# Kernel optimization log

Hardware: AMD Instinct MI355X
Metric: run time of the kernel (lower is better)

The kernel has to match this reference:

```python
import jax, jax.numpy as jnp
import numpy as np


def hard_sigmoid(x):
    # Theano/Keras hard_sigmoid: clip(0.2*x + 0.5, 0, 1)
    return jnp.clip(0.2 * x + 0.5, 0.0, 1.0)


def setup_inputs() -> dict:
    key = jax.random.key(0)
    ks = jax.random.split(key, 5)
    B, T, D, H = 64, 2048, 256, 128
    X = jax.random.normal(ks[0], (B, T, D), dtype=jnp.float32)
    W = jax.random.normal(ks[1], (D, H), dtype=jnp.float32) * 0.05
    U = jax.random.normal(ks[2], (H, H), dtype=jnp.float32) * (1.0 / np.sqrt(H))
    b = jnp.zeros((H,), dtype=jnp.float32)
    W_gate = jax.random.normal(ks[3], (D, H), dtype=jnp.float32) * 0.05
    b_gate = jnp.zeros((H,), dtype=jnp.float32)
    U_gate = jax.random.normal(ks[4], (H, H), dtype=jnp.float32) * (1.0 / np.sqrt(H))
    return {"X": X, "W": W, "U": U, "b": b,
            "W_gate": W_gate, "b_gate": b_gate, "U_gate": U_gate}


def reference(X, W, U, b, W_gate, b_gate, U_gate):
    # Precompute input projections for all timesteps (as the Theano code does)
    xx = jnp.einsum('btd,dh->bth', X, W) + b          # [B,T,H]
    xg = jnp.einsum('btd,dh->bth', X, W_gate) + b_gate  # [B,T,H]
    B, T, H = xx.shape

    def step(h, inp):
        xx_t, xg_t = inp                      # [B,H] each
        z = hard_sigmoid(xx_t + h @ U)        # update gate
        z_gate = jnp.tanh((xg_t * h) @ U_gate)
        z_out = jax.nn.softplus(h * z_gate)
        h_t = z * z_out + (1.0 - z) * h
        return h_t, None

    h0 = jnp.zeros((B, H), dtype=X.dtype)
    # scan over time: [T,B,H]
    h_final, _ = jax.lax.scan(step, h0, (jnp.swapaxes(xx, 0, 1), jnp.swapaxes(xg, 0, 1)))
    return h_final  # [B,H] (return_sequences=False -> last hidden state)
```

## Files before the change

### kernel.cpp

```cpp
#include <hip/hip_runtime.h>
#include <math.h>

#define B_ 64
#define T_ 2048
#define D_ 256
#define H_ 128

__device__ __forceinline__ float rlane(float v, int l) {
    return __int_as_float(__builtin_amdgcn_readlane(__float_as_int(v), l));
}
__device__ __forceinline__ float hard_sig(float x) {
    return fminf(fmaxf(fmaf(x, 0.2f, 0.5f), 0.0f), 1.0f);
}
__device__ __forceinline__ float fast_tanh(float x) {
    float ax = fabsf(x);
    float e  = __expf(-2.0f * ax);
    float r  = (1.0f - e) / (1.0f + e);
    return copysignf(r, x);
}
__device__ __forceinline__ float softplus_f(float x) {
    float ax = fabsf(x);
    return fmaxf(x, 0.0f) + __logf(1.0f + __expf(-ax));
}

__global__ __launch_bounds__(256) void proj_kernel(
    const float* __restrict__ X, const float* __restrict__ W,
    const float* __restrict__ Wg, const float* __restrict__ bias,
    const float* __restrict__ biasg, float* __restrict__ xxw,
    float* __restrict__ xgw, int t0, int Tc)
{
    const int tid = threadIdx.x;
    const int tx  = tid & 31;
    const int ty  = tid >> 5;
    const long rowbase = (long)blockIdx.x * 64;
    const int  b      = (int)(rowbase / Tc);
    const int  ttbase = (int)(rowbase % Tc);
    const float* xbase = X + ((long)b * T_ + t0 + ttbase) * D_;

    float accx[8][4];
    float accg[8][4];
#pragma unroll
    for (int r = 0; r < 8; ++r)
#pragma unroll
        for (int c = 0; c < 4; ++c) { accx[r][c] = 0.f; accg[r][c] = 0.f; }

    for (int k = 0; k < D_; k += 4) {
        float wA[4][4], wG[4][4];
#pragma unroll
        for (int kk = 0; kk < 4; ++kk) {
            float4 tw = *(const float4*)&W [(long)(k + kk) * H_ + tx * 4];
            float4 tg = *(const float4*)&Wg[(long)(k + kk) * H_ + tx * 4];
            wA[kk][0] = tw.x; wA[kk][1] = tw.y; wA[kk][2] = tw.z; wA[kk][3] = tw.w;
            wG[kk][0] = tg.x; wG[kk][1] = tg.y; wG[kk][2] = tg.z; wG[kk][3] = tg.w;
        }
#pragma unroll
        for (int r = 0; r < 8; ++r) {
            float4 xv = *(const float4*)&xbase[(long)(ty * 8 + r) * D_ + k];
            float xr[4] = {xv.x, xv.y, xv.z, xv.w};
#pragma unroll
            for (int c = 0; c < 4; ++c)
#pragma unroll
                for (int kk = 0; kk < 4; ++kk) {
                    accx[r][c] = fmaf(xr[kk], wA[kk][c], accx[r][c]);
                    accg[r][c] = fmaf(xr[kk], wG[kk][c], accg[r][c]);
                }
        }
    }

    float4 bj  = *(const float4*)&bias [tx * 4];
    float4 bgj = *(const float4*)&biasg[tx * 4];
#pragma unroll
    for (int r = 0; r < 8; ++r) {
        long row = rowbase + ty * 8 + r;
        float4 ox, og;
        ox.x = accx[r][0] + bj.x;  ox.y = accx[r][1] + bj.y;
        ox.z = accx[r][2] + bj.z;  ox.w = accx[r][3] + bj.w;
        og.x = accg[r][0] + bgj.x; og.y = accg[r][1] + bgj.y;
        og.z = accg[r][2] + bgj.z; og.w = accg[r][3] + bgj.w;
        *(float4*)&xxw[row * H_ + tx * 4] = ox;
        *(float4*)&xgw[row * H_ + tx * 4] = og;
    }
}

__global__ __launch_bounds__(512) void scan_kernel(
    const float* __restrict__ xxw, const float* __restrict__ xgw,
    const float* __restrict__ U, const float* __restrict__ Ug,
    float* __restrict__ hstate, float* __restrict__ hout,
    int t0, int Tc)
{
    const int tid    = threadIdx.x;
    const int j      = tid & 127;
    const int q      = tid >> 7;
    const int lane31 = tid & 31;
    const int i0     = q * 32;
    const int b      = blockIdx.x;

    __shared__ float hl[128];
    __shared__ float zp_l[4][128];
    __shared__ float gp_l[4][128];

    float Ureg[32], Ugreg[32];
#pragma unroll
    for (int i = 0; i < 32; ++i) {
        Ureg[i]  = U [(long)(i0 + i) * H_ + j];
        Ugreg[i] = Ug[(long)(i0 + i) * H_ + j];
    }

    const float* xxb = xxw + (long)b * Tc * H_;
    const float* xgb = xgw + (long)b * Tc * H_;

    float h0 = (t0 == 0) ? 0.0f : hstate[b * H_ + j];
    float hcur = h0;
    if (q == 0) hl[j] = h0;
    __syncthreads();

    float hbank  = hl[i0 + lane31];
    float xgbank = xgb[(long)0 * H_ + i0 + lane31];
    float abank  = xgbank * hbank;

    float xx_cur = xxb[j];
    int   t1     = (1 < Tc) ? 1 : Tc - 1;
    float xx_nxt = xxb[(long)t1 * H_ + j];
    float xgbank_nxt = xgb[(long)t1 * H_ + i0 + lane31];

    for (int t = 0; t < Tc; ++t) {
        float zp0 = 0.f, zp1 = 0.f, gp0 = 0.f, gp1 = 0.f;
#pragma unroll
        for (int i = 0; i < 32; i += 2) {
            float hs0 = rlane(hbank, i);
            float as0 = rlane(abank, i);
            float hs1 = rlane(hbank, i + 1);
            float as1 = rlane(abank, i + 1);
            zp0 = fmaf(hs0, Ureg[i],     zp0);
            gp0 = fmaf(as0, Ugreg[i],    gp0);
            zp1 = fmaf(hs1, Ureg[i + 1], zp1);
            gp1 = fmaf(as1, Ugreg[i + 1], gp1);
        }
        zp_l[q][j] = zp0 + zp1;
        gp_l[q][j] = gp0 + gp1;
        __syncthreads();

        if (tid < 256) {
            float zsum = xx_cur + zp_l[0][j] + zp_l[1][j] + zp_l[2][j] + zp_l[3][j];
            float gsum = gp_l[0][j] + gp_l[1][j] + gp_l[2][j] + gp_l[3][j];
            float z    = hard_sig(zsum);
            float zg   = fast_tanh(gsum);
            float zo   = softplus_f(hcur * zg);
            float hnew = fmaf(z, zo - hcur, hcur);
            if (q == 0) hl[j] = hnew;
            hcur = hnew;
        }
        __syncthreads();

        hbank  = hl[i0 + lane31];
        abank  = xgbank_nxt * hbank;
        xx_cur = xx_nxt;
        int t2 = (t + 2 < Tc) ? t + 2 : Tc - 1;
        xx_nxt     = xxb[(long)t2 * H_ + j];
        xgbank_nxt = xgb[(long)t2 * H_ + i0 + lane31];
    }

    if (q == 0) hout[b * H_ + j] = hcur;
}

extern "C" void kernel_launch(void* const* d_in, const int* in_sizes, int n_in,
                              void* d_out, int out_size, void* d_ws, size_t ws_size,
                              hipStream_t stream)
{
    const float* X  = (const float*)d_in[0];
    const float* W  = (const float*)d_in[1];
    const float* U  = (const float*)d_in[2];
    const float* bb = (const float*)d_in[3];
    const float* Wg = (const float*)d_in[4];
    const float* bg = (const float*)d_in[5];
    const float* Ug = (const float*)d_in[6];
    float* out = (float*)d_out;

    int Tc = 64;
    const int cands[6] = {2048, 1024, 512, 256, 128, 64};
    for (int ci = 0; ci < 6; ++ci) {
        size_t need = (size_t)2 * B_ * cands[ci] * H_ * sizeof(float)
                    + (size_t)B_ * H_ * sizeof(float);
        if (ws_size >= need) { Tc = cands[ci]; break; }
    }

    float* xxw = (float*)d_ws;
    float* xgw = xxw + (size_t)B_ * Tc * H_;
    float* hst = xgw + (size_t)B_ * Tc * H_;

    for (int t0 = 0; t0 < T_; t0 += Tc) {
        proj_kernel<<<B_ * Tc / 64, 256, 0, stream>>>(X, W, Wg, bb, bg, xxw, xgw, t0, Tc);
        float* ho = (t0 + Tc >= T_) ? out : hst;
        scan_kernel<<<B_, 512, 0, stream>>>(xxw, xgw, U, Ug, hst, ho, t0, Tc);
    }
}
```

Baseline: 1.883 ms.

## Restructure scan to one barrier per step with redundant epilogue; retile projection

```diff
diff --git a/kernel.cpp b/kernel.cpp
--- a/kernel.cpp
+++ b/kernel.cpp
@@ -6,16 +6,15 @@
 #define D_ 256
 #define H_ 128
 
-__device__ __forceinline__ float rlane(float v, int l) {
-    return __int_as_float(__builtin_amdgcn_readlane(__float_as_int(v), l));
-}
+typedef float v2f __attribute__((ext_vector_type(2)));
+
 __device__ __forceinline__ float hard_sig(float x) {
     return fminf(fmaxf(fmaf(x, 0.2f, 0.5f), 0.0f), 1.0f);
 }
 __device__ __forceinline__ float fast_tanh(float x) {
     float ax = fabsf(x);
     float e  = __expf(-2.0f * ax);
-    float r  = (1.0f - e) / (1.0f + e);
+    float r  = (1.0f - e) * __builtin_amdgcn_rcpf(1.0f + e);
     return copysignf(r, x);
 }
 __device__ __forceinline__ float softplus_f(float x) {
@@ -32,46 +31,87 @@
     const int tid = threadIdx.x;
     const int tx  = tid & 31;
     const int ty  = tid >> 5;
-    const long rowbase = (long)blockIdx.x * 64;
+    const long rowbase = (long)blockIdx.x * 32;
     const int  b      = (int)(rowbase / Tc);
     const int  ttbase = (int)(rowbase % Tc);
-    const float* xbase = X + ((long)b * T_ + t0 + ttbase) * D_;
-
-    float accx[8][4];
-    float accg[8][4];
-#pragma unroll
-    for (int r = 0; r < 8; ++r)
+    const float* xbase = X + ((long)b * T_ + t0 + ttbase + ty * 4) * D_;
+    const float* wp  = W  + tx * 4;
+    const float* wgp = Wg + tx * 4;
+
+    float accx[4][4], accg[4][4];
+#pragma unroll
+    for (int r = 0; r < 4; ++r)
 #pragma unroll
         for (int c = 0; c < 4; ++c) { accx[r][c] = 0.f; accg[r][c] = 0.f; }
 
-    for (int k = 0; k < D_; k += 4) {
-        float wA[4][4], wG[4][4];
+    float4 xA[4], xB[4];
+    float4 wWA[4], wGA[4], wWB[4], wGB[4];
+
+#pragma unroll
+    for (int r = 0; r < 4; ++r) xA[r] = *(const float4*)&xbase[(long)r * D_];
+#pragma unroll
+    for (int kk = 0; kk < 4; ++kk) {
+        wWA[kk] = *(const float4*)&wp [(long)kk * H_];
+        wGA[kk] = *(const float4*)&wgp[(long)kk * H_];
+    }
+
+#pragma unroll 1
+    for (int kc = 0; kc < 64; kc += 2) {
+        const int kB  = (kc + 1) * 4;
+        const int kA2 = (kc + 2 < 64) ? (kc + 2) * 4 : kB;
+
+#pragma unroll
+        for (int r = 0; r < 4; ++r) xB[r] = *(const float4*)&xbase[(long)r * D_ + kB];
 #pragma unroll
         for (int kk = 0; kk < 4; ++kk) {
-            float4 tw = *(const float4*)&W [(long)(k + kk) * H_ + tx * 4];
-            float4 tg = *(const float4*)&Wg[(long)(k + kk) * H_ + tx * 4];
-            wA[kk][0] = tw.x; wA[kk][1] = tw.y; wA[kk][2] = tw.z; wA[kk][3] = tw.w;
-            wG[kk][0] = tg.x; wG[kk][1] = tg.y; wG[kk][2] = tg.z; wG[kk][3] = tg.w;
-        }
-#pragma unroll
-        for (int r = 0; r < 8; ++r) {
-            float4 xv = *(const float4*)&xbase[(long)(ty * 8 + r) * D_ + k];
-            float xr[4] = {xv.x, xv.y, xv.z, xv.w};
-#pragma unroll
-            for (int c = 0; c < 4; ++c)
-#pragma unroll
-                for (int kk = 0; kk < 4; ++kk) {
-                    accx[r][c] = fmaf(xr[kk], wA[kk][c], accx[r][c]);
-                    accg[r][c] = fmaf(xr[kk], wG[kk][c], accg[r][c]);
-                }
+            wWB[kk] = *(const float4*)&wp [(long)(kB + kk) * H_];
+            wGB[kk] = *(const float4*)&wgp[(long)(kB + kk) * H_];
+        }
+#pragma unroll
+        for (int r = 0; r < 4; ++r) {
+            const float xr[4] = {xA[r].x, xA[r].y, xA[r].z, xA[r].w};
+#pragma unroll
+            for (int kk = 0; kk < 4; ++kk) {
+                accx[r][0] = fmaf(xr[kk], wWA[kk].x, accx[r][0]);
+                accx[r][1] = fmaf(xr[kk], wWA[kk].y, accx[r][1]);
+                accx[r][2] = fmaf(xr[kk], wWA[kk].z, accx[r][2]);
+                accx[r][3] = fmaf(xr[kk], wWA[kk].w, accx[r][3]);
+                accg[r][0] = fmaf(xr[kk], wGA[kk].x, accg[r][0]);
+                accg[r][1] = fmaf(xr[kk], wGA[kk].y, accg[r][1]);
+                accg[r][2] = fmaf(xr[kk], wGA[kk].z, accg[r][2]);
+                accg[r][3] = fmaf(xr[kk], wGA[kk].w, accg[r][3]);
+            }
+        }
+
+#pragma unroll
+        for (int r = 0; r < 4; ++r) xA[r] = *(const float4*)&xbase[(long)r * D_ + kA2];
+#pragma unroll
+        for (int kk = 0; kk < 4; ++kk) {
+            wWA[kk] = *(const float4*)&wp [(long)(kA2 + kk) * H_];
+            wGA[kk] = *(const float4*)&wgp[(long)(kA2 + kk) * H_];
+        }
+#pragma unroll
+        for (int r = 0; r < 4; ++r) {
+            const float xr[4] = {xB[r].x, xB[r].y, xB[r].z, xB[r].w};
+#pragma unroll
+            for (int kk = 0; kk < 4; ++kk) {
+                accx[r][0] = fmaf(xr[kk], wWB[kk].x, accx[r][0]);
+                accx[r][1] = fmaf(xr[kk], wWB[kk].y, accx[r][1]);
+                accx[r][2] = fmaf(xr[kk], wWB[kk].z, accx[r][2]);
+                accx[r][3] = fmaf(xr[kk], wWB[kk].w, accx[r][3]);
+                accg[r][0] = fmaf(xr[kk], wGB[kk].x, accg[r][0]);
+                accg[r][1] = fmaf(xr[kk], wGB[kk].y, accg[r][1]);
+                accg[r][2] = fmaf(xr[kk], wGB[kk].z, accg[r][2]);
+                accg[r][3] = fmaf(xr[kk], wGB[kk].w, accg[r][3]);
+            }
         }
     }
 
     float4 bj  = *(const float4*)&bias [tx * 4];
     float4 bgj = *(const float4*)&biasg[tx * 4];
 #pragma unroll
-    for (int r = 0; r < 8; ++r) {
-        long row = rowbase + ty * 8 + r;
+    for (int r = 0; r < 4; ++r) {
+        long row = rowbase + ty * 4 + r;
         float4 ox, og;
         ox.x = accx[r][0] + bj.x;  ox.y = accx[r][1] + bj.y;
         ox.z = accx[r][2] + bj.z;  ox.w = accx[r][3] + bj.w;
@@ -88,79 +128,89 @@
     float* __restrict__ hstate, float* __restrict__ hout,
     int t0, int Tc)
 {
-    const int tid    = threadIdx.x;
-    const int j      = tid & 127;
-    const int q      = tid >> 7;
-    const int lane31 = tid & 31;
-    const int i0     = q * 32;
-    const int b      = blockIdx.x;
-
-    __shared__ float hl[128];
-    __shared__ float zp_l[4][128];
-    __shared__ float gp_l[4][128];
-
-    float Ureg[32], Ugreg[32];
-#pragma unroll
-    for (int i = 0; i < 32; ++i) {
-        Ureg[i]  = U [(long)(i0 + i) * H_ + j];
-        Ugreg[i] = Ug[(long)(i0 + i) * H_ + j];
+    const int tid = threadIdx.x;
+    const int jp  = tid & 63;
+    const int q   = tid >> 6;
+    const int i0  = q * 16;
+    const int jj  = i0 + (tid & 15);
+    const int b   = blockIdx.x;
+
+    __shared__ v2f zb[2][8][64];
+    __shared__ v2f gb[2][8][64];
+
+    v2f Up[16], Ugp[16];
+#pragma unroll
+    for (int i = 0; i < 16; ++i) {
+        Up[i]  = *(const v2f*)&U [(long)(i0 + i) * H_ + 2 * jp];
+        Ugp[i] = *(const v2f*)&Ug[(long)(i0 + i) * H_ + 2 * jp];
+    }
+#pragma unroll
+    for (int i = 0; i < 16; ++i) {
+        asm volatile("" : "+v"(Up[i]));
+        asm volatile("" : "+v"(Ugp[i]));
     }
 
     const float* xxb = xxw + (long)b * Tc * H_;
     const float* xgb = xgw + (long)b * Tc * H_;
 
-    float h0 = (t0 == 0) ? 0.0f : hstate[b * H_ + j];
-    float hcur = h0;
-    if (q == 0) hl[j] = h0;
-    __syncthreads();
-
-    float hbank  = hl[i0 + lane31];
-    float xgbank = xgb[(long)0 * H_ + i0 + lane31];
-    float abank  = xgbank * hbank;
-
-    float xx_cur = xxb[j];
-    int   t1     = (1 < Tc) ? 1 : Tc - 1;
-    float xx_nxt = xxb[(long)t1 * H_ + j];
-    float xgbank_nxt = xgb[(long)t1 * H_ + i0 + lane31];
+    float hbank = (t0 == 0) ? 0.0f : hstate[b * H_ + jj];
+    float abank = xgb[jj] * hbank;
+
+    const int t1i = (Tc > 1) ? 1 : 0;
+    float xxc = xxb[jj];
+    float xx1 = xxb[(long)t1i * H_ + jj];
+    float xg1 = xgb[(long)t1i * H_ + jj];
 
     for (int t = 0; t < Tc; ++t) {
-        float zp0 = 0.f, zp1 = 0.f, gp0 = 0.f, gp1 = 0.f;
-#pragma unroll
-        for (int i = 0; i < 32; i += 2) {
-            float hs0 = rlane(hbank, i);
-            float as0 = rlane(abank, i);
-            float hs1 = rlane(hbank, i + 1);
-            float as1 = rlane(abank, i + 1);
-            zp0 = fmaf(hs0, Ureg[i],     zp0);
-            gp0 = fmaf(as0, Ugreg[i],    gp0);
-            zp1 = fmaf(hs1, Ureg[i + 1], zp1);
-            gp1 = fmaf(as1, Ugreg[i + 1], gp1);
-        }
-        zp_l[q][j] = zp0 + zp1;
-        gp_l[q][j] = gp0 + gp1;
-        __syncthreads();
-
-        if (tid < 256) {
-            float zsum = xx_cur + zp_l[0][j] + zp_l[1][j] + zp_l[2][j] + zp_l[3][j];
-            float gsum = gp_l[0][j] + gp_l[1][j] + gp_l[2][j] + gp_l[3][j];
-            float z    = hard_sig(zsum);
-            float zg   = fast_tanh(gsum);
-            float zo   = softplus_f(hcur * zg);
-            float hnew = fmaf(z, zo - hcur, hcur);
-            if (q == 0) hl[j] = hnew;
-            hcur = hnew;
-        }
-        __syncthreads();
-
-        hbank  = hl[i0 + lane31];
-        abank  = xgbank_nxt * hbank;
-        xx_cur = xx_nxt;
-        int t2 = (t + 2 < Tc) ? t + 2 : Tc - 1;
-        xx_nxt     = xxb[(long)t2 * H_ + j];
-        xgbank_nxt = xgb[(long)t2 * H_ + i0 + lane31];
-    }
-
-    if (q == 0) hout[b * H_ + j] = hcur;
+        int tp = t + 2; if (tp >= Tc) tp = Tc - 1;
+        float xx2 = xxb[(long)tp * H_ + jj];
+        float xg2 = xgb[(long)tp * H_ + jj];
+
+        v2f zpA = {0.f, 0.f}, zpB = {0.f, 0.f};
+        v2f gpA = {0.f, 0.f}, gpB = {0.f, 0.f};
+        const int hb = __float_as_int(hbank);
+        const int ab = __float_as_int(abank);
+#pragma unroll
+        for (int i = 0; i < 16; i += 2) {
+            const float h0 = __int_as_float(__builtin_amdgcn_readlane(hb, i));
+            const float a0 = __int_as_float(__builtin_amdgcn_readlane(ab, i));
+            const float h1 = __int_as_float(__builtin_amdgcn_readlane(hb, i + 1));
+            const float a1 = __int_as_float(__builtin_amdgcn_readlane(ab, i + 1));
+            zpA.x = fmaf(h0, Up[i].x,      zpA.x);
+            zpA.y = fmaf(h0, Up[i].y,      zpA.y);
+            gpA.x = fmaf(a0, Ugp[i].x,     gpA.x);
+            gpA.y = fmaf(a0, Ugp[i].y,     gpA.y);
+            zpB.x = fmaf(h1, Up[i + 1].x,  zpB.x);
+            zpB.y = fmaf(h1, Up[i + 1].y,  zpB.y);
+            gpB.x = fmaf(a1, Ugp[i + 1].x, gpB.x);
+            gpB.y = fmaf(a1, Ugp[i + 1].y, gpB.y);
+        }
+        const int buf = t & 1;
+        zb[buf][q][jp] = zpA + zpB;
+        gb[buf][q][jp] = gpA + gpB;
+
+        asm volatile("s_waitcnt lgkmcnt(0)" ::: "memory");
+        __builtin_amdgcn_s_barrier();
+        asm volatile("" ::: "memory");
+
+        const float* zf = (const float*)&zb[buf][0][0];
+        const float* gf = (const float*)&gb[buf][0][0];
+        float zsum = xxc, gsum = 0.f;
+#pragma unroll
+        for (int s = 0; s < 8; ++s) {
+            zsum += zf[s * 128 + jj];
+            gsum += gf[s * 128 + jj];
+        }
+        float z    = hard_sig(zsum);
+        float zg   = fast_tanh(gsum);
+        float zo   = softplus_f(hbank * zg);
+        float hnew = fmaf(z, zo - hbank, hbank);
+        hbank = hnew;
+        abank = xg1 * hnew;
+        xxc = xx1; xx1 = xx2; xg1 = xg2;
+    }
+
+    if ((tid & 63) < 16) hout[b * H_ + jj] = hbank;
 }
 
 extern "C" void kernel_launch(void* const* d_in, const int* in_sizes, int n_in,
@@ -189,7 +239,7 @@
     float* hst = xgw + (size_t)B_ * Tc * H_;
 
     for (int t0 = 0; t0 < T_; t0 += Tc) {
-        proj_kernel<<<B_ * Tc / 64, 256, 0, stream>>>(X, W, Wg, bb, bg, xxw, xgw, t0, Tc);
+        proj_kernel<<<B_ * Tc / 32, 256, 0, stream>>>(X, W, Wg, bb, bg, xxw, xgw, t0, Tc);
         float* ho = (t0 + Tc >= T_) ? out : hst;
         scan_kernel<<<B_, 512, 0, stream>>>(xxw, xgw, U, Ug, hst, ho, t0, Tc);
     }
```

Measured after the change: 1.788 ms. 1.05x faster.
